# Optimization experiments

Hardware: AMD Instinct MI355X
Metric: run time of the kernel (lower is better)

The kernel has to match this reference:

```python
import jax, jax.numpy as jnp
import numpy as np

NUM_CP = 32

def setup_inputs() -> dict:
    key = jax.random.key(0)
    kx, kc = jax.random.split(key)
    x = jax.random.normal(kx, (64, 1048576), dtype=jnp.float32)
    control_points = jax.random.normal(kc, (NUM_CP,), dtype=jnp.float32) / np.sqrt(NUM_CP).astype(np.float32)
    knots = jnp.linspace(0.0, 1.0, NUM_CP, dtype=jnp.float32)
    return {"x": x, "control_points": control_points, "knots": knots}

def reference(x, control_points, knots):
    # normalize x to [0, ~1) exactly like the torch module
    xn = (x - x.min()) / (x.max() - x.min() + 1e-6)
    n = knots.shape[0]
    # bucketize: bin index i such that knots[i] <= xn < knots[i+1]
    # (points exactly on an interior knot give t=0 in the right bin, which equals
    idx = jnp.clip(jnp.searchsorted(knots, xn, side='right') - 1, 0, n - 2)
    k0 = knots[idx]
    k1 = knots[idx + 1]
    t = (xn - k0) / (k1 - k0)
    out = (1.0 - t) * control_points[idx] + t * control_points[idx + 1]
    # torch loop leaves points outside [knots[0], knots[-1]] at zero
    in_range = (xn >= knots[0]) & (xn <= knots[-1])
    return jnp.where(in_range, out, jnp.zeros((), dtype=out.dtype))
```

## Files before the change

### kernel.cpp

```cpp
#include <hip/hip_runtime.h>
#include <hip/hip_cooperative_groups.h>

namespace cg = cooperative_groups;

typedef float vf4 __attribute__((ext_vector_type(4)));

#define NB 1024
#define NT 256

__device__ __forceinline__ void nt_store4(float4* p, float4 v) {
    __builtin_nontemporal_store(*reinterpret_cast<vf4*>(&v), reinterpret_cast<vf4*>(p));
}
__device__ __forceinline__ float4 nt_load4(const float4* p) {
    vf4 t = __builtin_nontemporal_load(reinterpret_cast<const vf4*>(p));
    float4 r; r.x = t.x; r.y = t.y; r.z = t.z; r.w = t.w;
    return r;
}

__device__ __forceinline__ void block_minmax(float& mn, float& mx,
                                             volatile float* smn, volatile float* smx) {
    #pragma unroll
    for (int off = 32; off > 0; off >>= 1) {
        mn = fminf(mn, __shfl_down(mn, off, 64));
        mx = fmaxf(mx, __shfl_down(mx, off, 64));
    }
    int wave = threadIdx.x >> 6;
    int lane = threadIdx.x & 63;
    if (lane == 0) { smn[wave] = mn; smx[wave] = mx; }
    __syncthreads();
    if (threadIdx.x == 0) {
        #pragma unroll
        for (int w = 1; w < NT / 64; ++w) {
            mn = fminf(mn, smn[w]);
            mx = fmaxf(mx, smx[w]);
        }
    }
}

__device__ __forceinline__ float spline_eval(float xv, float mn, float scale,
                                             const float* sk, const float* sa,
                                             const float* sb, float klo, float khi) {
    float xn = (xv - mn) * scale;
    int b = (int)(xn * 31.0f);
    b = b < 0 ? 0 : (b > 30 ? 30 : b);
    if (xn < sk[b]) {
        b = (b > 0) ? b - 1 : 0;
    } else if (xn >= sk[b + 1]) {
        b = (b < 30) ? b + 1 : 30;
    }
    float val = fmaf(xn - sk[b], sb[b], sa[b]);
    return (xn >= klo && xn <= khi) ? val : 0.0f;
}

__global__ __launch_bounds__(NT, 4) void spline_fused(const float4* __restrict__ x,
                                                      const float* __restrict__ cp,
                                                      const float* __restrict__ knots,
                                                      float* __restrict__ ws,
                                                      float4* __restrict__ out, int n4) {
    __shared__ float sk[32];
    __shared__ float sa[32];
    __shared__ float sb[32];
    __shared__ float smn[NT / 64], smx[NT / 64];
    __shared__ float sbc[2];

    if (threadIdx.x < 32) {
        sk[threadIdx.x] = knots[threadIdx.x];
        sa[threadIdx.x] = cp[threadIdx.x];
    }
    __syncthreads();
    if (threadIdx.x < 31) {
        int i = threadIdx.x;
        sb[i] = (sa[i + 1] - sa[i]) / (sk[i + 1] - sk[i]);
    }

    const int gtid   = blockIdx.x * NT + threadIdx.x;
    const int stride = NB * NT;

    float mn = INFINITY, mx = -INFINITY;
    int i = gtid;
    for (; i + stride < n4; i += 2 * stride) {
        float4 a = x[i];
        float4 b = x[i + stride];
        mn = fminf(mn, fminf(fminf(a.x, a.y), fminf(a.z, a.w)));
        mx = fmaxf(mx, fmaxf(fmaxf(a.x, a.y), fmaxf(a.z, a.w)));
        mn = fminf(mn, fminf(fminf(b.x, b.y), fminf(b.z, b.w)));
        mx = fmaxf(mx, fmaxf(fmaxf(b.x, b.y), fmaxf(b.z, b.w)));
    }
    for (; i < n4; i += stride) {
        float4 a = x[i];
        mn = fminf(mn, fminf(fminf(a.x, a.y), fminf(a.z, a.w)));
        mx = fmaxf(mx, fmaxf(fmaxf(a.x, a.y), fmaxf(a.z, a.w)));
    }
    block_minmax(mn, mx, smn, smx);
    if (threadIdx.x == 0) {
        __hip_atomic_store(&ws[blockIdx.x],      mn, __ATOMIC_RELAXED, __HIP_MEMORY_SCOPE_AGENT);
        __hip_atomic_store(&ws[NB + blockIdx.x], mx, __ATOMIC_RELAXED, __HIP_MEMORY_SCOPE_AGENT);
        __threadfence();
    }

    cg::this_grid().sync();

    mn = INFINITY; mx = -INFINITY;
    for (int j = threadIdx.x; j < NB; j += NT) {
        mn = fminf(mn, __hip_atomic_load(&ws[j],      __ATOMIC_RELAXED, __HIP_MEMORY_SCOPE_AGENT));
        mx = fmaxf(mx, __hip_atomic_load(&ws[NB + j], __ATOMIC_RELAXED, __HIP_MEMORY_SCOPE_AGENT));
    }
    block_minmax(mn, mx, smn, smx);
    if (threadIdx.x == 0) { sbc[0] = mn; sbc[1] = mx; }
    __syncthreads();
    mn = sbc[0]; mx = sbc[1];

    const float scale = 1.0f / (mx - mn + 1e-6f);
    const float klo = sk[0], khi = sk[31];

    const int KMAX = (n4 + stride - 1) / stride;
    int k = KMAX - 1;
    for (; k >= 1; k -= 2) {
        const int i0 = k * stride + gtid;
        const int i1 = (k - 1) * stride + gtid;
        const bool ok0 = (i0 < n4);
        float4 v0 = ok0 ? nt_load4(&x[i0]) : make_float4(0.f, 0.f, 0.f, 0.f);
        float4 v1 = nt_load4(&x[i1]);
        float4 r0, r1;
        r0.x = spline_eval(v0.x, mn, scale, sk, sa, sb, klo, khi);
        r0.y = spline_eval(v0.y, mn, scale, sk, sa, sb, klo, khi);
        r0.z = spline_eval(v0.z, mn, scale, sk, sa, sb, klo, khi);
        r0.w = spline_eval(v0.w, mn, scale, sk, sa, sb, klo, khi);
        r1.x = spline_eval(v1.x, mn, scale, sk, sa, sb, klo, khi);
        r1.y = spline_eval(v1.y, mn, scale, sk, sa, sb, klo, khi);
        r1.z = spline_eval(v1.z, mn, scale, sk, sa, sb, klo, khi);
        r1.w = spline_eval(v1.w, mn, scale, sk, sa, sb, klo, khi);
        if (ok0) nt_store4(&out[i0], r0);
        nt_store4(&out[i1], r1);
    }
    if (k == 0) {
        const int i0 = gtid;
        if (i0 < n4) {
            float4 v0 = nt_load4(&x[i0]);
            float4 r0;
            r0.x = spline_eval(v0.x, mn, scale, sk, sa, sb, klo, khi);
            r0.y = spline_eval(v0.y, mn, scale, sk, sa, sb, klo, khi);
            r0.z = spline_eval(v0.z, mn, scale, sk, sa, sb, klo, khi);
            r0.w = spline_eval(v0.w, mn, scale, sk, sa, sb, klo, khi);
            nt_store4(&out[i0], r0);
        }
    }
}

extern "C" void kernel_launch(void* const* d_in, const int* in_sizes, int n_in,
                              void* d_out, int out_size, void* d_ws, size_t ws_size,
                              hipStream_t stream) {
    const float4* x     = (const float4*)d_in[0];
    const float*  cp    = (const float*)d_in[1];
    const float*  knots = (const float*)d_in[2];
    float*  ws  = (float*)d_ws;
    float4* out = (float4*)d_out;

    int n  = in_sizes[0];
    int n4 = n / 4;

    void* args[] = {(void*)&x, (void*)&cp, (void*)&knots, (void*)&ws, (void*)&out, (void*)&n4};
    hipLaunchCooperativeKernel((const void*)spline_fused, dim3(NB), dim3(NT), args, 0, stream);
}
```

Baseline: 636.5 us.

## Double cooperative grid, unroll loops by four, add non-cooperative fallback path

Raises the cooperative grid from 1024 to 2048 blocks with launch bounds of 8 blocks per CU, so more waves are resident to hide memory latency. The min/max and spline passes are unrolled to four float4 loads per iteration, with a peel loop so the apply pass still walks backwards through cache-resident data. It also adds a two-kernel fallback (atomic ordered-int min/max, then apply) for when the workspace is too small or the cooperative launch fails. The higher occupancy target may force register spilling, and the grid barrier now has to synchronise more blocks.

```diff
diff --git a/kernel.cpp b/kernel.cpp
--- a/kernel.cpp
+++ b/kernel.cpp
@@ -3,9 +3,10 @@
 
 namespace cg = cooperative_groups;
 
+typedef unsigned int u32;
 typedef float vf4 __attribute__((ext_vector_type(4)));
 
-#define NB 1024
+#define NB 2048
 #define NT 256
 
 __device__ __forceinline__ void nt_store4(float4* p, float4 v) {
@@ -15,6 +16,11 @@
     vf4 t = __builtin_nontemporal_load(reinterpret_cast<const vf4*>(p));
     float4 r; r.x = t.x; r.y = t.y; r.z = t.z; r.w = t.w;
     return r;
+}
+
+__device__ __forceinline__ void mm4(float4 v, float& mn, float& mx) {
+    mn = fminf(mn, fminf(fminf(v.x, v.y), fminf(v.z, v.w)));
+    mx = fmaxf(mx, fmaxf(fmaxf(v.x, v.y), fmaxf(v.z, v.w)));
 }
 
 __device__ __forceinline__ void block_minmax(float& mn, float& mx,
@@ -52,7 +58,7 @@
     return (xn >= klo && xn <= khi) ? val : 0.0f;
 }
 
-__global__ __launch_bounds__(NT, 4) void spline_fused(const float4* __restrict__ x,
+__global__ __launch_bounds__(NT, 8) void spline_fused(const float4* __restrict__ x,
                                                       const float* __restrict__ cp,
                                                       const float* __restrict__ knots,
                                                       float* __restrict__ ws,
@@ -73,37 +79,36 @@
         sb[i] = (sa[i + 1] - sa[i]) / (sk[i + 1] - sk[i]);
     }
 
+    const int nb     = gridDim.x;
     const int gtid   = blockIdx.x * NT + threadIdx.x;
-    const int stride = NB * NT;
+    const int stride = nb * NT;
 
     float mn = INFINITY, mx = -INFINITY;
     int i = gtid;
-    for (; i + stride < n4; i += 2 * stride) {
+    for (; i + 3 * stride < n4; i += 4 * stride) {
         float4 a = x[i];
         float4 b = x[i + stride];
-        mn = fminf(mn, fminf(fminf(a.x, a.y), fminf(a.z, a.w)));
-        mx = fmaxf(mx, fmaxf(fmaxf(a.x, a.y), fmaxf(a.z, a.w)));
-        mn = fminf(mn, fminf(fminf(b.x, b.y), fminf(b.z, b.w)));
-        mx = fmaxf(mx, fmaxf(fmaxf(b.x, b.y), fmaxf(b.z, b.w)));
+        float4 c = x[i + 2 * stride];
+        float4 d = x[i + 3 * stride];
+        mm4(a, mn, mx); mm4(b, mn, mx); mm4(c, mn, mx); mm4(d, mn, mx);
     }
     for (; i < n4; i += stride) {
         float4 a = x[i];
-        mn = fminf(mn, fminf(fminf(a.x, a.y), fminf(a.z, a.w)));
-        mx = fmaxf(mx, fmaxf(fmaxf(a.x, a.y), fmaxf(a.z, a.w)));
+        mm4(a, mn, mx);
     }
     block_minmax(mn, mx, smn, smx);
     if (threadIdx.x == 0) {
         __hip_atomic_store(&ws[blockIdx.x],      mn, __ATOMIC_RELAXED, __HIP_MEMORY_SCOPE_AGENT);
-        __hip_atomic_store(&ws[NB + blockIdx.x], mx, __ATOMIC_RELAXED, __HIP_MEMORY_SCOPE_AGENT);
+        __hip_atomic_store(&ws[nb + blockIdx.x], mx, __ATOMIC_RELAXED, __HIP_MEMORY_SCOPE_AGENT);
         __threadfence();
     }
 
     cg::this_grid().sync();
 
     mn = INFINITY; mx = -INFINITY;
-    for (int j = threadIdx.x; j < NB; j += NT) {
+    for (int j = threadIdx.x; j < nb; j += NT) {
         mn = fminf(mn, __hip_atomic_load(&ws[j],      __ATOMIC_RELAXED, __HIP_MEMORY_SCOPE_AGENT));
-        mx = fmaxf(mx, __hip_atomic_load(&ws[NB + j], __ATOMIC_RELAXED, __HIP_MEMORY_SCOPE_AGENT));
+        mx = fmaxf(mx, __hip_atomic_load(&ws[nb + j], __ATOMIC_RELAXED, __HIP_MEMORY_SCOPE_AGENT));
     }
     block_minmax(mn, mx, smn, smx);
     if (threadIdx.x == 0) { sbc[0] = mn; sbc[1] = mx; }
@@ -115,35 +120,127 @@
 
     const int KMAX = (n4 + stride - 1) / stride;
     int k = KMAX - 1;
-    for (; k >= 1; k -= 2) {
-        const int i0 = k * stride + gtid;
-        const int i1 = (k - 1) * stride + gtid;
-        const bool ok0 = (i0 < n4);
-        float4 v0 = ok0 ? nt_load4(&x[i0]) : make_float4(0.f, 0.f, 0.f, 0.f);
+    while (k >= 0 && ((k + 1) & 3)) {
+        const int idx = k * stride + gtid;
+        if (idx < n4) {
+            float4 v = nt_load4(&x[idx]);
+            float4 r;
+            r.x = spline_eval(v.x, mn, scale, sk, sa, sb, klo, khi);
+            r.y = spline_eval(v.y, mn, scale, sk, sa, sb, klo, khi);
+            r.z = spline_eval(v.z, mn, scale, sk, sa, sb, klo, khi);
+            r.w = spline_eval(v.w, mn, scale, sk, sa, sb, klo, khi);
+            nt_store4(&out[idx], r);
+        }
+        --k;
+    }
+    for (; k >= 3; k -= 4) {
+        const int i3 = k * stride + gtid;
+        const int i2 = i3 - stride;
+        const int i1 = i2 - stride;
+        const int i0 = i1 - stride;
+        const bool ok3 = (i3 < n4);
+        float4 v3 = ok3 ? nt_load4(&x[i3]) : make_float4(0.f, 0.f, 0.f, 0.f);
+        float4 v2 = nt_load4(&x[i2]);
         float4 v1 = nt_load4(&x[i1]);
-        float4 r0, r1;
+        float4 v0 = nt_load4(&x[i0]);
+        float4 r0, r1, r2, r3;
+        r3.x = spline_eval(v3.x, mn, scale, sk, sa, sb, klo, khi);
+        r3.y = spline_eval(v3.y, mn, scale, sk, sa, sb, klo, khi);
+        r3.z = spline_eval(v3.z, mn, scale, sk, sa, sb, klo, khi);
+        r3.w = spline_eval(v3.w, mn, scale, sk, sa, sb, klo, khi);
+        r2.x = spline_eval(v2.x, mn, scale, sk, sa, sb, klo, khi);
+        r2.y = spline_eval(v2.y, mn, scale, sk, sa, sb, klo, khi);
+        r2.z = spline_eval(v2.z, mn, scale, sk, sa, sb, klo, khi);
+        r2.w = spline_eval(v2.w, mn, scale, sk, sa, sb, klo, khi);
+        r1.x = spline_eval(v1.x, mn, scale, sk, sa, sb, klo, khi);
+        r1.y = spline_eval(v1.y, mn, scale, sk, sa, sb, klo, khi);
+        r1.z = spline_eval(v1.z, mn, scale, sk, sa, sb, klo, khi);
+        r1.w = spline_eval(v1.w, mn, scale, sk, sa, sb, klo, khi);
         r0.x = spline_eval(v0.x, mn, scale, sk, sa, sb, klo, khi);
         r0.y = spline_eval(v0.y, mn, scale, sk, sa, sb, klo, khi);
         r0.z = spline_eval(v0.z, mn, scale, sk, sa, sb, klo, khi);
         r0.w = spline_eval(v0.w, mn, scale, sk, sa, sb, klo, khi);
-        r1.x = spline_eval(v1.x, mn, scale, sk, sa, sb, klo, khi);
-        r1.y = spline_eval(v1.y, mn, scale, sk, sa, sb, klo, khi);
-        r1.z = spline_eval(v1.z, mn, scale, sk, sa, sb, klo, khi);
-        r1.w = spline_eval(v1.w, mn, scale, sk, sa, sb, klo, khi);
-        if (ok0) nt_store4(&out[i0], r0);
+        if (ok3) nt_store4(&out[i3], r3);
+        nt_store4(&out[i2], r2);
         nt_store4(&out[i1], r1);
-    }
-    if (k == 0) {
-        const int i0 = gtid;
-        if (i0 < n4) {
-            float4 v0 = nt_load4(&x[i0]);
-            float4 r0;
-            r0.x = spline_eval(v0.x, mn, scale, sk, sa, sb, klo, khi);
-            r0.y = spline_eval(v0.y, mn, scale, sk, sa, sb, klo, khi);
-            r0.z = spline_eval(v0.z, mn, scale, sk, sa, sb, klo, khi);
-            r0.w = spline_eval(v0.w, mn, scale, sk, sa, sb, klo, khi);
-            nt_store4(&out[i0], r0);
-        }
+        nt_store4(&out[i0], r0);
+    }
+}
+
+
+__device__ __forceinline__ u32 f2ord(float f) {
+    u32 b = __float_as_uint(f);
+    return (b & 0x80000000u) ? ~b : (b | 0x80000000u);
+}
+__device__ __forceinline__ float ord2f(u32 k) {
+    u32 b = (k & 0x80000000u) ? (k ^ 0x80000000u) : ~k;
+    return __uint_as_float(b);
+}
+
+__global__ __launch_bounds__(256) void minmax_kernel(const float4* __restrict__ x, int n4,
+                                                     u32* __restrict__ ws) {
+    float mn = INFINITY, mx = -INFINITY;
+    int stride = gridDim.x * blockDim.x;
+    for (int i = blockIdx.x * blockDim.x + threadIdx.x; i < n4; i += stride) {
+        float4 v = x[i];
+        mm4(v, mn, mx);
+    }
+    #pragma unroll
+    for (int off = 32; off > 0; off >>= 1) {
+        mn = fminf(mn, __shfl_down(mn, off, 64));
+        mx = fmaxf(mx, __shfl_down(mx, off, 64));
+    }
+    __shared__ float smn[4], smx[4];
+    int wave = threadIdx.x >> 6;
+    int lane = threadIdx.x & 63;
+    if (lane == 0) { smn[wave] = mn; smx[wave] = mx; }
+    __syncthreads();
+    if (threadIdx.x == 0) {
+        #pragma unroll
+        for (int w = 1; w < 4; ++w) { mn = fminf(mn, smn[w]); mx = fmaxf(mx, smx[w]); }
+        atomicMax(&ws[0], ~f2ord(mn));
+        atomicMax(&ws[1],  f2ord(mx));
+    }
+}
+
+__global__ __launch_bounds__(256) void apply_kernel(const float4* __restrict__ x,
+                                                    const float* __restrict__ cp,
+                                                    const float* __restrict__ knots,
+                                                    const u32* __restrict__ ws,
+                                                    float4* __restrict__ out, int n4) {
+    __shared__ float sk[32];
+    __shared__ float sa[32];
+    __shared__ float sb[32];
+    if (threadIdx.x < 32) {
+        sk[threadIdx.x] = knots[threadIdx.x];
+        sa[threadIdx.x] = cp[threadIdx.x];
+    }
+    __syncthreads();
+    if (threadIdx.x < 31) {
+        int i = threadIdx.x;
+        sb[i] = (sa[i + 1] - sa[i]) / (sk[i + 1] - sk[i]);
+    }
+    __syncthreads();
+
+    float mn = ord2f(~ws[0]);
+    float mx = ord2f(ws[1]);
+    float scale = 1.0f / (mx - mn + 1e-6f);
+    float klo = sk[0], khi = sk[31];
+
+    const int gtid   = blockIdx.x * blockDim.x + threadIdx.x;
+    const int stride = gridDim.x * blockDim.x;
+    const int KMAX   = (n4 + stride - 1) / stride;
+
+    for (int k = KMAX - 1; k >= 0; --k) {
+        const int i = k * stride + gtid;
+        if (i >= n4) continue;
+        float4 v = nt_load4(&x[i]);
+        float4 r;
+        r.x = spline_eval(v.x, mn, scale, sk, sa, sb, klo, khi);
+        r.y = spline_eval(v.y, mn, scale, sk, sa, sb, klo, khi);
+        r.z = spline_eval(v.z, mn, scale, sk, sa, sb, klo, khi);
+        r.w = spline_eval(v.w, mn, scale, sk, sa, sb, klo, khi);
+        nt_store4(&out[i], r);
     }
 }
 
@@ -153,12 +250,22 @@
     const float4* x     = (const float4*)d_in[0];
     const float*  cp    = (const float*)d_in[1];
     const float*  knots = (const float*)d_in[2];
-    float*  ws  = (float*)d_ws;
     float4* out = (float4*)d_out;
 
     int n  = in_sizes[0];
     int n4 = n / 4;
 
-    void* args[] = {(void*)&x, (void*)&cp, (void*)&knots, (void*)&ws, (void*)&out, (void*)&n4};
-    hipLaunchCooperativeKernel((const void*)spline_fused, dim3(NB), dim3(NT), args, 0, stream);
-}
+    bool fused_ok = (ws_size >= (size_t)(2 * NB) * sizeof(float));
+    if (fused_ok) {
+        float* ws = (float*)d_ws;
+        void* args[] = {(void*)&x, (void*)&cp, (void*)&knots, (void*)&ws, (void*)&out, (void*)&n4};
+        hipError_t e = hipLaunchCooperativeKernel((const void*)spline_fused,
+                                                  dim3(NB), dim3(NT), args, 0, stream);
+        if (e == hipSuccess) return;
+    }
+
+    u32* ws32 = (u32*)d_ws;
+    hipMemsetAsync(ws32, 0x00, 8, stream);
+    minmax_kernel<<<4096, 256, 0, stream>>>(x, n4, ws32);
+    apply_kernel <<<8192, 256, 0, stream>>>(x, cp, knots, ws32, out, n4);
+}
```

Result: slower. 909.9 us (+42.9%).
